# Performance work log

Hardware: AMD Instinct MI355X
Metric: run time of the kernel (lower is better)

The kernel has to match this reference:

```python
import jax, jax.numpy as jnp
import numpy as np

B_, T_, TS, DE, H, LD, OD = 16, 4096, 64, 128, 256, 512, 10
RMIN, RMAX, MAXPH = 0.9, 0.999, 6.283
EPS = 1e-5
NBLK = 6


def setup_inputs() -> dict:
    key = jax.random.key(0)
    ks = jax.random.split(key, 14)
    x = jax.random.normal(ks[0], (B_, T_, TS), jnp.float32)
    # LRU ring init (Orvieto et al.)
    u1 = jax.random.uniform(ks[1], (NBLK, H))
    u2 = jax.random.uniform(ks[2], (NBLK, H))
    nu_log = jnp.log(-0.5 * jnp.log(u1 * (RMAX**2 - RMIN**2) + RMIN**2))
    theta_log = jnp.log(MAXPH * u2)
    B_re = jax.random.normal(ks[3], (NBLK, H, DE)) / np.sqrt(2 * DE)
    B_im = jax.random.normal(ks[4], (NBLK, H, DE)) / np.sqrt(2 * DE)
    C_re = jax.random.normal(ks[5], (NBLK, DE, H)) / np.sqrt(H)
    C_im = jax.random.normal(ks[6], (NBLK, DE, H)) / np.sqrt(H)
    D_lru = jax.random.normal(ks[7], (NBLK, DE))
    W1 = jax.random.normal(ks[8], (NBLK, DE, LD)) / np.sqrt(DE)
    b1 = jnp.zeros((NBLK, LD))
    W2 = jax.random.normal(ks[9], (NBLK, LD // 2, DE)) / np.sqrt(LD // 2)
    b2 = jnp.zeros((NBLK, DE))
    bn_scale = jnp.ones((NBLK, DE))
    bn_bias = jnp.zeros((NBLK, DE))
    W_enc = jax.random.normal(ks[10], (TS, DE)) / np.sqrt(TS)
    b_enc = jnp.zeros((DE,))
    W_out = jax.random.normal(ks[11], (DE, OD)) / np.sqrt(DE)
    b_out = jnp.zeros((OD,))
    return dict(x=x, nu_log=nu_log, theta_log=theta_log, B_re=B_re, B_im=B_im,
                C_re=C_re, C_im=C_im, D_lru=D_lru, W1=W1, b1=b1, W2=W2, b2=b2,
                bn_scale=bn_scale, bn_bias=bn_bias, W_enc=W_enc, b_enc=b_enc,
                W_out=W_out, b_out=b_out)


def _lru(u, nu_log_i, theta_log_i, Bre, Bim, Cre, Cim, Dv):
    # u: [B,T,DE] float. Diagonal complex linear recurrence via associative scan.
    lam = jnp.exp(-jnp.exp(nu_log_i) + 1j * jnp.exp(theta_log_i))        # [H]
    gamma = jnp.sqrt(jnp.clip(1.0 - jnp.abs(lam) ** 2, 1e-8, None))      # [H]
    Bc = (Bre + 1j * Bim) * gamma[:, None]                               # [H,DE]
    Bu = jnp.einsum('btd,hd->bth', u.astype(jnp.complex64), Bc)          # [B,T,H]
    lam_b = jnp.broadcast_to(lam, Bu.shape)

    def binop(a, b):
        return (a[0] * b[0], a[1] * b[0] + b[1])

    _, h = jax.lax.associative_scan(binop, (lam_b, Bu), axis=1)          # [B,T,H]
    y = jnp.einsum('bth,dh->btd', h, Cre + 1j * Cim).real + u * Dv
    return y


def _bn(x, scale, bias):
    # training-mode batchnorm over (batch, time) with feature axis last
    m = x.mean(axis=(0, 1))
    v = x.var(axis=(0, 1))
    return (x - m) * jax.lax.rsqrt(v + EPS) * scale + bias


def reference(x, nu_log, theta_log, B_re, B_im, C_re, C_im, D_lru,
              W1, b1, W2, b2, bn_scale, bn_bias, W_enc, b_enc, W_out, b_out):
    h = x @ W_enc + b_enc                       # [B,T,DE]
    y = h
    for i in range(NBLK):
        z = _bn(h, bn_scale[i], bn_bias[i])
        z = _lru(z, nu_log[i], theta_log[i], B_re[i], B_im[i], C_re[i], C_im[i], D_lru[i])
        z = z @ W1[i] + b1[i]                   # [B,T,LD]
        a, b = jnp.split(z, 2, axis=-1)
        z = a * jax.nn.sigmoid(b)               # GLU
        z = z @ W2[i] + b2[i]                   # [B,T,DE]
        h = z + y                               # residual to encoder output
    pooled = h.mean(axis=1)                     # pool=True: mean over tokens
    return pooled @ W_out + b_out               # [B,OD]
```

## Files before the change

kernel.cpp:

```cpp
#include <hip/hip_runtime.h>
#include <hip/hip_fp16.h>

#define BB 16
#define TT 4096
#define TSZ 64
#define DE 128
#define HH 256
#define LDIM 512
#define ODIM 10
#define NBLKS 6
#define EPSF 1e-5f
#define NC32 128
#define NC64 64
#define NROWS (BB*TT)

typedef _Float16 f16x8 __attribute__((ext_vector_type(8)));
typedef _Float16 f16x4 __attribute__((ext_vector_type(4)));
typedef float f32x4 __attribute__((ext_vector_type(4)));
#define MFMA16(a,b,c) __builtin_amdgcn_mfma_f32_16x16x32_f16((a),(b),(c),0,0,0)

enum : size_t {
  HOFF_BG = 0,
  HOFF_WC = HOFF_BG + (size_t)NBLKS*512*128,
  HOFF_W1 = HOFF_WC + (size_t)NBLKS*128*512,
  HOFF_W2 = HOFF_W1 + (size_t)NBLKS*512*128,
  HOFF_WE = HOFF_W2 + (size_t)NBLKS*128*256,
  HTOT_HALFS = HOFF_WE + 128*64
};

enum : size_t {
  WOFF_Y     = 0,
  WOFF_H     = WOFF_Y + (size_t)NROWS*DE/2,
  WOFF_W16   = WOFF_H + (size_t)NROWS*DE/2,
  WOFF_LAM   = WOFF_W16 + (HTOT_HALFS+1)/2,
  WOFF_LAML  = WOFF_LAM + (size_t)NBLKS*HH*2,
  WOFF_SL    = WOFF_LAML + (size_t)NBLKS*HH*2,
  WOFF_CARRY = WOFF_SL + (size_t)BB*NC32*HH*2,
  WOFF_STATS = WOFF_CARRY + (size_t)BB*NC32*HH*2,
  WOFF_POOL  = WOFF_STATS + (size_t)(NBLKS+1)*2*DE,
  WOFF_BU    = WOFF_POOL + (size_t)BB*DE,
  WS_FLOATS  = WOFF_BU + (size_t)BB*NC32*512*32/2
};

__global__ __launch_bounds__(256) void k_prep(
    const float* __restrict__ nu_log, const float* __restrict__ theta_log,
    const float* __restrict__ B_re, const float* __restrict__ B_im,
    const float* __restrict__ C_re, const float* __restrict__ C_im,
    const float* __restrict__ W1g, const float* __restrict__ W2g,
    const float* __restrict__ Wenc, float* __restrict__ ws)
{
  const int i = blockIdx.x, h = threadIdx.x;
  __half* w16 = (__half*)(ws + WOFF_W16);
  const float nu  = expf(nu_log[i*HH+h]);
  const float th  = expf(theta_log[i*HH+h]);
  const float mod = expf(-nu);
  const float lr = mod*cosf(th), li = mod*sinf(th);
  const float gamma = sqrtf(fmaxf(1.0f - mod*mod, 1e-8f));
  ws[WOFF_LAM + ((size_t)i*HH+h)*2+0] = lr;
  ws[WOFF_LAM + ((size_t)i*HH+h)*2+1] = li;
  {
    float ar = lr, ai = li;
    #pragma unroll
    for (int q = 0; q < 5; q++) { float nr=ar*ar-ai*ai, ni=2.0f*ar*ai; ar=nr; ai=ni; }
    ws[WOFF_LAML + ((size_t)i*HH+h)*2+0] = ar;
    ws[WOFF_LAML + ((size_t)i*HH+h)*2+1] = ai;
  }
  {
    __half* bg = w16 + HOFF_BG + (size_t)i*512*128;
    const float* bre = B_re + ((size_t)i*HH+h)*DE;
    const float* bim = B_im + ((size_t)i*HH+h)*DE;
    for (int d = 0; d < DE; d++) {
      bg[(size_t)h*128 + d]       = __float2half(bre[d]*gamma);
      bg[(size_t)(256+h)*128 + d] = __float2half(bim[d]*gamma);
    }
  }
  {
    __half* wc = w16 + HOFF_WC + (size_t)i*128*512;
    const float* cre = C_re + (size_t)i*DE*HH;
    const float* cim = C_im + (size_t)i*DE*HH;
    for (int d = 0; d < DE; d++) {
      wc[(size_t)d*512 + h]       = __float2half( cre[(size_t)d*HH + h]);
      wc[(size_t)d*512 + 256 + h] = __float2half(-cim[(size_t)d*HH + h]);
    }
  }
  {
    __half* w1t = w16 + HOFF_W1 + (size_t)i*512*128;
    for (int d = 0; d < DE; d++) {
      w1t[(size_t)h*128 + d]       = __float2half(W1g[((size_t)i*DE + d)*LDIM + h]);
      w1t[(size_t)(256+h)*128 + d] = __float2half(W1g[((size_t)i*DE + d)*LDIM + 256 + h]);
    }
  }
  if (h < 128) {
    __half* w2t = w16 + HOFF_W2 + (size_t)i*128*256;
    for (int g = 0; g < 256; g++)
      w2t[(size_t)h*256 + g] = __float2half(W2g[((size_t)i*256 + g)*DE + h]);
  }
  if (i == 0 && h < 128) {
    __half* wet = w16 + HOFF_WE;
    for (int k = 0; k < TSZ; k++)
      wet[(size_t)h*TSZ + k] = __float2half(Wenc[(size_t)k*DE + h]);
  }
}

__global__ __launch_bounds__(512) void k_enc(
    const float* __restrict__ x, const float* __restrict__ benc, float* __restrict__ ws)
{
  __shared__ __half XT[64*72];
  const int tid = threadIdx.x, w = tid >> 6, l = tid & 63;
  const size_t row0 = (size_t)blockIdx.x * 64;
  {
    const float4* xg = (const float4*)(x + row0*TSZ);
    for (int idx = tid; idx < 1024; idx += 512) {
      float4 v = xg[idx];
      const int r = idx >> 4, c4 = (idx & 15)*4;
      *(__half2*)&XT[r*72 + c4]     = __half2{__float2half(v.x), __float2half(v.y)};
      *(__half2*)&XT[r*72 + c4 + 2] = __half2{__float2half(v.z), __float2half(v.w)};
    }
  }
  __syncthreads();
  const __half* wet = (const __half*)(ws + WOFF_W16) + HOFF_WE;
  const int n0 = w*16;
  f32x4 acc[4];
  #pragma unroll
  for (int mt = 0; mt < 4; mt++) acc[mt] = (f32x4)(0.0f);
  #pragma unroll
  for (int k0 = 0; k0 < 64; k0 += 32) {
    f16x8 bf = *(const f16x8*)&wet[(size_t)(n0 + (l&15))*64 + k0 + (l>>4)*8];
    #pragma unroll
    for (int mt = 0; mt < 4; mt++) {
      f16x8 af = *(const f16x8*)&XT[(mt*16 + (l&15))*72 + k0 + (l>>4)*8];
      acc[mt] = MFMA16(af, bf, acc[mt]);
    }
  }
  const int d = n0 + (l&15);
  const float be = benc[d];
  float s = 0.0f, ss = 0.0f;
  __half* y = (__half*)(ws + WOFF_Y);
  #pragma unroll
  for (int mt = 0; mt < 4; mt++)
    #pragma unroll
    for (int j = 0; j < 4; j++) {
      const int t = mt*16 + (l>>4)*4 + j;
      const float v = acc[mt][j] + be;
      y[(row0 + t)*DE + d] = __float2half(v);
      s += v; ss += v*v;
    }
  s  += __shfl_xor(s, 16);  s  += __shfl_xor(s, 32);
  ss += __shfl_xor(ss, 16); ss += __shfl_xor(ss, 32);
  if (l < 16) {
    atomicAdd(ws + WOFF_STATS + d, s);
    atomicAdd(ws + WOFF_STATS + DE + d, ss);
  }
}

__global__ __launch_bounds__(512, 4) void k_A(
    const __half* __restrict__ hin, float* __restrict__ ws,
    const float* __restrict__ bnsg, const float* __restrict__ bnbg, int iblk)
{
  __shared__ float AC[256];
  __shared__ __half U[64*136];
  const int tid = threadIdx.x, w = tid >> 6, l = tid & 63, q = l >> 4, r = l & 15;
  const int b = blockIdx.y, cb = blockIdx.x;
  const int row0 = b*TT + cb*64;
  if (tid < 128) {
    const float inv = 1.0f / (float)NROWS;
    const float s  = ws[WOFF_STATS + ((size_t)iblk*2+0)*DE + tid];
    const float sq = ws[WOFF_STATS + ((size_t)iblk*2+1)*DE + tid];
    const float mean = s*inv;
    const float var  = sq*inv - mean*mean;
    const float a = rsqrtf(var + EPSF) * bnsg[iblk*DE + tid];
    AC[tid]       = a;
    AC[128 + tid] = bnbg[iblk*DE + tid] - mean*a;
  }
  __syncthreads();
  {
    const int row = tid >> 3, d0 = (tid & 7)*16;
    const f16x8* hp = (const f16x8*)(hin + (size_t)(row0+row)*DE + d0);
    f16x8 h0 = hp[0], h1 = hp[1];
    f16x8 u0, u1;
    #pragma unroll
    for (int j = 0; j < 8; j++) {
      u0[j] = (_Float16)((float)h0[j]*AC[d0+j]   + AC[128+d0+j]);
      u1[j] = (_Float16)((float)h1[j]*AC[d0+8+j] + AC[128+d0+8+j]);
    }
    *(f16x8*)&U[row*136 + d0]     = u0;
    *(f16x8*)&U[row*136 + d0 + 8] = u1;
  }
  __syncthreads();
  const __half* BG = (const __half*)(ws + WOFF_W16) + HOFF_BG + (size_t)iblk*512*128;
  const int n0 = w*64;
  f32x4 acc[4][4];
  #pragma unroll
  for (int mt = 0; mt < 4; mt++)
    #pragma unroll
    for (int nt = 0; nt < 4; nt++) acc[mt][nt] = (f32x4)(0.0f);
  #pragma unroll
  for (int k0 = 0; k0 < 128; k0 += 32) {
    f16x8 af[4], bf[4];
    #pragma unroll
    for (int mt = 0; mt < 4; mt++)
      af[mt] = *(const f16x8*)&U[(mt*16 + r)*136 + k0 + q*8];
    #pragma unroll
    for (int nt = 0; nt < 4; nt++)
      bf[nt] = *(const f16x8*)&BG[(size_t)(n0 + nt*16 + r)*128 + k0 + q*8];
    #pragma unroll
    for (int mt = 0; mt < 4; mt++)
      #pragma unroll
      for (int nt = 0; nt < 4; nt++)
        acc[mt][nt] = MFMA16(af[mt], bf[nt], acc[mt][nt]);
  }
  __half* bu = (__half*)(ws + WOFF_BU);
  #pragma unroll
  for (int mt = 0; mt < 4; mt++)
    #pragma unroll
    for (int nt = 0; nt < 4; nt++) {
      f16x4 pk;
      pk[0] = (_Float16)acc[mt][nt][0];
      pk[1] = (_Float16)acc[mt][nt][1];
      pk[2] = (_Float16)acc[mt][nt][2];
      pk[3] = (_Float16)acc[mt][nt][3];
      const int hc = n0 + nt*16 + r;
      __half* dst = bu + ((((size_t)b*NC32 + cb*2 + (mt>>1))*512 + hc)*32 + (mt&1)*16 + q*4);
      *(f16x4*)dst = pk;
    }
}

__global__ __launch_bounds__(256) void k_pre(float* __restrict__ ws, int iblk)
{
  const int h = threadIdx.x, c = blockIdx.x, b = blockIdx.y;
  const __half* bu = (const __half*)(ws + WOFF_BU) + ((size_t)(b*NC32 + c)*512)*32;
  f16x8 re[4], im[4];
  #pragma unroll
  for (int k = 0; k < 4; k++) {
    re[k] = *(const f16x8*)(bu + (size_t)h*32 + k*8);
    im[k] = *(const f16x8*)(bu + (size_t)(256+h)*32 + k*8);
  }
  const float lr = ws[WOFF_LAM + ((size_t)iblk*HH+h)*2+0];
  const float li = ws[WOFF_LAM + ((size_t)iblk*HH+h)*2+1];
  float sr = 0.0f, si = 0.0f;
  #pragma unroll
  for (int t = 0; t < 32; t++) {
    const float br = (float)re[t>>3][t&7];
    const float bi = (float)im[t>>3][t&7];
    const float nr = lr*sr - li*si + br;
    const float ni = lr*si + li*sr + bi;
    sr = nr; si = ni;
  }
  ws[WOFF_SL + ((size_t)(b*NC32+c)*HH + h)*2+0] = sr;
  ws[WOFF_SL + ((size_t)(b*NC32+c)*HH + h)*2+1] = si;
}

__global__ void k_carry(float* __restrict__ ws, int i)
{
  const int h = threadIdx.x;
  const int b = blockIdx.x;
  const float Lr = ws[WOFF_LAML + ((size_t)i*HH+h)*2+0];
  const float Li = ws[WOFF_LAML + ((size_t)i*HH+h)*2+1];
  float2* C = (float2*)(ws + WOFF_CARRY) + (size_t)b*NC32*HH + h;
  const float2* S = (const float2*)(ws + WOFF_SL) + (size_t)b*NC32*HH + h;
  float sr = 0.0f, si = 0.0f;
  C[0] = float2{0.0f, 0.0f};
  for (int c = 1; c < NC32; c++) {
    const float2 sl = S[(size_t)(c-1)*HH];
    const float nr = Lr*sr - Li*si + sl.x;
    const float ni = Lr*si + Li*sr + sl.y;
    sr = nr; si = ni;
    C[(size_t)c*HH] = float2{sr, si};
  }
}

__global__ __launch_bounds__(512, 4) void k_BC(
    const __half* __restrict__ hin, float* __restrict__ ws,
    const float* __restrict__ bnsg, const float* __restrict__ bnbg,
    const float* __restrict__ b1g, const float* __restrict__ b2g,
    const float* __restrict__ Dvg, int iblk, int islast)
{
  __shared__ __half HT[64*264];
  __shared__ __half YL[64*136];
  __shared__ float AC[256];
  __shared__ float DVs[128];
  const int tid = threadIdx.x, w = tid >> 6, l = tid & 63, q = l >> 4, r = l & 15;
  const int b = blockIdx.y, cb = blockIdx.x;
  const int row0 = b*TT + cb*64;
  const __half* w16 = (const __half*)(ws + WOFF_W16);

  if (tid < 128) {
    const float inv = 1.0f / (float)NROWS;
    const float s  = ws[WOFF_STATS + ((size_t)iblk*2+0)*DE + tid];
    const float sq = ws[WOFF_STATS + ((size_t)iblk*2+1)*DE + tid];
    const float mean = s*inv;
    const float var  = sq*inv - mean*mean;
    const float a = rsqrtf(var + EPSF) * bnsg[iblk*DE + tid];
    AC[tid]       = a;
    AC[128 + tid] = bnbg[iblk*DE + tid] - mean*a;
    DVs[tid] = Dvg[iblk*DE + tid];
  }

  __half2 simv[16];
  {
    const int h = tid & 255, p = tid >> 8;
    const int c32 = cb*2 + p;
    const float2 carry = *((const float2*)(ws + WOFF_CARRY) + ((size_t)b*NC32 + c32)*HH + h);
    const __half* bu = (const __half*)(ws + WOFF_BU) + ((size_t)(b*NC32 + c32)*512)*32;
    f16x8 re[4], im[4];
    #pragma unroll
    for (int k = 0; k < 4; k++) {
      re[k] = *(const f16x8*)(bu + (size_t)h*32 + k*8);
      im[k] = *(const f16x8*)(bu + (size_t)(256+h)*32 + k*8);
    }
    const float lr = ws[WOFF_LAM + ((size_t)iblk*HH+h)*2+0];
    const float li = ws[WOFF_LAM + ((size_t)iblk*HH+h)*2+1];
    float sr = carry.x, si = carry.y;
    #pragma unroll
    for (int t = 0; t < 32; t++) {
      const float br = (float)re[t>>3][t&7];
      const float bi = (float)im[t>>3][t&7];
      const float nr = lr*sr - li*si + br;
      const float ni = lr*si + li*sr + bi;
      sr = nr; si = ni;
      HT[(p*32 + t)*264 + h] = __float2half(sr);
      if ((t & 1) == 0) simv[t>>1].x = __float2half(si);
      else              simv[t>>1].y = __float2half(si);
    }
  }
  __syncthreads();

  const __half* WC = w16 + HOFF_WC + (size_t)iblk*128*512;
  const int d = w*16 + r;
  f32x4 acc2[4];
  #pragma unroll
  for (int mt = 0; mt < 4; mt++) acc2[mt] = (f32x4)(0.0f);
  #pragma unroll
  for (int k0 = 0; k0 < 256; k0 += 32) {
    f16x8 bf = *(const f16x8*)&WC[(size_t)d*512 + k0 + q*8];
    #pragma unroll
    for (int mt = 0; mt < 4; mt++) {
      f16x8 af = *(const f16x8*)&HT[(mt*16 + r)*264 + k0 + q*8];
      acc2[mt] = MFMA16(af, bf, acc2[mt]);
    }
  }
  __syncthreads();
  {
    const int h = tid & 255, p = tid >> 8;
    #pragma unroll
    for (int t = 0; t < 32; t++)
      HT[(p*32 + t)*264 + h] = ((t & 1) ? simv[t>>1].y : simv[t>>1].x);
  }
  __syncthreads();
  #pragma unroll
  for (int k0 = 0; k0 < 256; k0 += 32) {
    f16x8 bf = *(const f16x8*)&WC[(size_t)d*512 + 256 + k0 + q*8];
    #pragma unroll
    for (int mt = 0; mt < 4; mt++) {
      f16x8 af = *(const f16x8*)&HT[(mt*16 + r)*264 + k0 + q*8];
      acc2[mt] = MFMA16(af, bf, acc2[mt]);
    }
  }
  {
    const float dv = DVs[d], a = AC[d], c = AC[128+d];
    #pragma unroll
    for (int mt = 0; mt < 4; mt++)
      #pragma unroll
      for (int j = 0; j < 4; j++) {
        const int t = mt*16 + q*4 + j;
        const float u = (float)hin[(size_t)(row0+t)*DE + d]*a + c;
        YL[t*136 + d] = __float2half(acc2[mt][j] + u*dv);
      }
  }
  __syncthreads();

  {
    const __half* W1T = w16 + HOFF_W1 + (size_t)iblk*512*128;
    #pragma unroll
    for (int nt = 0; nt < 2; nt++) {
      const int ca = w*32 + nt*16 + r;
      f32x4 aa[4], ab[4];
      #pragma unroll
      for (int mt = 0; mt < 4; mt++) { aa[mt] = (f32x4)(0.0f); ab[mt] = (f32x4)(0.0f); }
      #pragma unroll
      for (int k0 = 0; k0 < 128; k0 += 32) {
        f16x8 ba = *(const f16x8*)&W1T[(size_t)ca*128 + k0 + q*8];
        f16x8 bb = *(const f16x8*)&W1T[(size_t)(256+ca)*128 + k0 + q*8];
        #pragma unroll
        for (int mt = 0; mt < 4; mt++) {
          f16x8 af = *(const f16x8*)&YL[(mt*16 + r)*136 + k0 + q*8];
          aa[mt] = MFMA16(af, ba, aa[mt]);
          ab[mt] = MFMA16(af, bb, ab[mt]);
        }
      }
      const float b1a = b1g[(size_t)iblk*LDIM + ca];
      const float b1b = b1g[(size_t)iblk*LDIM + 256 + ca];
      #pragma unroll
      for (int mt = 0; mt < 4; mt++)
        #pragma unroll
        for (int j = 0; j < 4; j++) {
          const int t = mt*16 + q*4 + j;
          const float av = aa[mt][j] + b1a;
          const float bv = ab[mt][j] + b1b;
          HT[t*264 + ca] = __float2half(av / (1.0f + __expf(-bv)));
        }
    }
  }
  __syncthreads();

  {
    const __half* W2T = w16 + HOFF_W2 + (size_t)iblk*128*256;
    f32x4 ac4[4];
    #pragma unroll
    for (int mt = 0; mt < 4; mt++) ac4[mt] = (f32x4)(0.0f);
    #pragma unroll
    for (int k0 = 0; k0 < 256; k0 += 32) {
      f16x8 bf = *(const f16x8*)&W2T[(size_t)d*256 + k0 + q*8];
      #pragma unroll
      for (int mt = 0; mt < 4; mt++) {
        f16x8 af = *(const f16x8*)&HT[(mt*16 + r)*264 + k0 + q*8];
        ac4[mt] = MFMA16(af, bf, ac4[mt]);
      }
    }
    const __half* yh = (const __half*)(ws + WOFF_Y);
    __half* hh = (__half*)(ws + WOFF_H);
    const float bb2 = b2g[(size_t)iblk*DE + d];
    float s = 0.0f, ss = 0.0f;
    #pragma unroll
    for (int mt = 0; mt < 4; mt++)
      #pragma unroll
      for (int j = 0; j < 4; j++) {
        const int t = mt*16 + q*4 + j;
        const size_t row = (size_t)(row0 + t);
        const float v = ac4[mt][j] + bb2 + (float)yh[row*DE + d];
        hh[row*DE + d] = __float2half(v);
        s += v; ss += v*v;
      }
    s  += __shfl_xor(s, 16);  s  += __shfl_xor(s, 32);
    ss += __shfl_xor(ss, 16); ss += __shfl_xor(ss, 32);
    if (l < 16) {
      atomicAdd(ws + WOFF_STATS + (size_t)((iblk+1)*2 + 0)*DE + d, s);
      atomicAdd(ws + WOFF_STATS + (size_t)((iblk+1)*2 + 1)*DE + d, ss);
      if (islast) atomicAdd(ws + WOFF_POOL + (size_t)b*DE + d, s);
    }
  }
}

__global__ void k_out(const float* __restrict__ Wout, const float* __restrict__ bout,
                      const float* __restrict__ ws, float* __restrict__ out)
{
  const int tid = threadIdx.x;
  if (tid < BB*ODIM) {
    const int b = tid / ODIM, o = tid % ODIM;
    float acc = bout[o];
    const float* p = ws + WOFF_POOL + (size_t)b*DE;
    const float invT = 1.0f / (float)TT;
    for (int d = 0; d < DE; d++) acc += p[d]*invT*Wout[d*ODIM + o];
    out[tid] = acc;
  }
}

extern "C" void kernel_launch(void* const* d_in, const int* in_sizes, int n_in,
                              void* d_out, int out_size, void* d_ws, size_t ws_size,
                              hipStream_t stream)
{
  const float* x   = (const float*)d_in[0];
  const float* nu  = (const float*)d_in[1];
  const float* th  = (const float*)d_in[2];
  const float* Bre = (const float*)d_in[3];
  const float* Bim = (const float*)d_in[4];
  const float* Cre = (const float*)d_in[5];
  const float* Cim = (const float*)d_in[6];
  const float* Dv  = (const float*)d_in[7];
  const float* W1  = (const float*)d_in[8];
  const float* b1  = (const float*)d_in[9];
  const float* W2  = (const float*)d_in[10];
  const float* b2  = (const float*)d_in[11];
  const float* bns = (const float*)d_in[12];
  const float* bnb = (const float*)d_in[13];
  const float* We  = (const float*)d_in[14];
  const float* be  = (const float*)d_in[15];
  const float* Wo  = (const float*)d_in[16];
  const float* bo  = (const float*)d_in[17];
  float* ws = (float*)d_ws;
  float* out = (float*)d_out;

  hipMemsetAsync(ws + WOFF_STATS, 0,
                 (size_t)(((NBLKS+1)*2*DE) + BB*DE)*sizeof(float), stream);

  k_prep<<<NBLKS, 256, 0, stream>>>(nu, th, Bre, Bim, Cre, Cim, W1, W2, We, ws);
  k_enc<<<NROWS/64, 512, 0, stream>>>(x, be, ws);

  const __half* Yh = (const __half*)(ws + WOFF_Y);
  const __half* Hh = (const __half*)(ws + WOFF_H);
  for (int i = 0; i < NBLKS; i++) {
    const __half* hin = (i == 0) ? Yh : Hh;
    k_A    <<<dim3(NC64, BB), 512, 0, stream>>>(hin, ws, bns, bnb, i);
    k_pre  <<<dim3(NC32, BB), 256, 0, stream>>>(ws, i);
    k_carry<<<BB, 256, 0, stream>>>(ws, i);
    k_BC   <<<dim3(NC64, BB), 512, 0, stream>>>(hin, ws, bns, bnb, b1, b2, Dv, i,
                                                (i == NBLKS-1) ? 1 : 0);
  }
  k_out<<<1, 256, 0, stream>>>(Wo, bo, ws, out);
}
```

Before: 958.8 us.

## Fuse chunk-local scan sums into k_A via lambda powers; halve k_BC tile

Drops the k_pre kernel. Each 32-step chunk's local scan endpoint is now computed inside k_A as a weighted sum of the MFMA outputs with precomputed lambda powers (lambda^(31-tau)), using cross-lane shuffles and a shared-memory reduction. k_BC now processes 32 rows per block instead of 64, with twice as many blocks and occupancy hint 6. It runs the real and imaginary halves of the state as one K=512 MFMA pass instead of two passes with an LDS rewrite, and prefetches inputs early. This saves a launch and a BU reread, at the cost of extra FMA and register work in k_A, different fp32 summation order, and more blocks reloading weights.

```diff
diff --git a/kernel.cpp b/kernel.cpp
--- a/kernel.cpp
+++ b/kernel.cpp
@@ -34,7 +34,8 @@
   WOFF_W16   = WOFF_H + (size_t)NROWS*DE/2,
   WOFF_LAM   = WOFF_W16 + (HTOT_HALFS+1)/2,
   WOFF_LAML  = WOFF_LAM + (size_t)NBLKS*HH*2,
-  WOFF_SL    = WOFF_LAML + (size_t)NBLKS*HH*2,
+  WOFF_PL32  = WOFF_LAML + (size_t)NBLKS*HH*2,
+  WOFF_SL    = WOFF_PL32 + (size_t)NBLKS*32*HH*2,
   WOFF_CARRY = WOFF_SL + (size_t)BB*NC32*HH*2,
   WOFF_STATS = WOFF_CARRY + (size_t)BB*NC32*HH*2,
   WOFF_POOL  = WOFF_STATS + (size_t)(NBLKS+1)*2*DE,
@@ -66,6 +67,17 @@
     ws[WOFF_LAML + ((size_t)i*HH+h)*2+1] = ai;
   }
   {
+    float pr = 1.0f, pi = 0.0f;
+    float* P = ws + WOFF_PL32 + (size_t)i*32*HH*2;
+    for (int j = 0; j < 32; j++) {
+      const int tau = 31 - j;
+      P[((size_t)tau*HH + h)*2+0] = pr;
+      P[((size_t)tau*HH + h)*2+1] = pi;
+      const float nr = pr*lr - pi*li, ni = pr*li + pi*lr;
+      pr = nr; pi = ni;
+    }
+  }
+  {
     __half* bg = w16 + HOFF_BG + (size_t)i*512*128;
     const float* bre = B_re + ((size_t)i*HH+h)*DE;
     const float* bim = B_im + ((size_t)i*HH+h)*DE;
@@ -159,6 +171,7 @@
 {
   __shared__ float AC[256];
   __shared__ __half U[64*136];
+  __shared__ float SC[2][2][256][2];
   const int tid = threadIdx.x, w = tid >> 6, l = tid & 63, q = l >> 4, r = l & 15;
   const int b = blockIdx.y, cb = blockIdx.x;
   const int row0 = b*TT + cb*64;
@@ -223,31 +236,51 @@
       __half* dst = bu + ((((size_t)b*NC32 + cb*2 + (mt>>1))*512 + hc)*32 + (mt&1)*16 + q*4);
       *(f16x4*)dst = pk;
     }
-}
-
-__global__ __launch_bounds__(256) void k_pre(float* __restrict__ ws, int iblk)
-{
-  const int h = threadIdx.x, c = blockIdx.x, b = blockIdx.y;
-  const __half* bu = (const __half*)(ws + WOFF_BU) + ((size_t)(b*NC32 + c)*512)*32;
-  f16x8 re[4], im[4];
-  #pragma unroll
-  for (int k = 0; k < 4; k++) {
-    re[k] = *(const f16x8*)(bu + (size_t)h*32 + k*8);
-    im[k] = *(const f16x8*)(bu + (size_t)(256+h)*32 + k*8);
-  }
-  const float lr = ws[WOFF_LAM + ((size_t)iblk*HH+h)*2+0];
-  const float li = ws[WOFF_LAM + ((size_t)iblk*HH+h)*2+1];
-  float sr = 0.0f, si = 0.0f;
-  #pragma unroll
-  for (int t = 0; t < 32; t++) {
-    const float br = (float)re[t>>3][t&7];
-    const float bi = (float)im[t>>3][t&7];
-    const float nr = lr*sr - li*si + br;
-    const float ni = lr*si + li*sr + bi;
-    sr = nr; si = ni;
-  }
-  ws[WOFF_SL + ((size_t)(b*NC32+c)*HH + h)*2+0] = sr;
-  ws[WOFF_SL + ((size_t)(b*NC32+c)*HH + h)*2+1] = si;
+  {
+    const float2* PW = (const float2*)(ws + WOFF_PL32) + (size_t)iblk*32*HH;
+    float ppr[2][4], ppi[2][4];
+    #pragma unroll
+    for (int cc = 0; cc < 2; cc++)
+      #pragma unroll
+      for (int nt = 0; nt < 4; nt++) { ppr[cc][nt] = 0.0f; ppi[cc][nt] = 0.0f; }
+    #pragma unroll
+    for (int mm = 0; mm < 2; mm++)
+      #pragma unroll
+      for (int j = 0; j < 4; j++) {
+        const int tau = mm*16 + q*4 + j;
+        #pragma unroll
+        for (int nt = 0; nt < 4; nt++) {
+          const int hcol = (w&3)*64 + nt*16 + r;
+          const float2 pw = PW[(size_t)tau*HH + hcol];
+          #pragma unroll
+          for (int cc = 0; cc < 2; cc++) {
+            const float v = acc[cc*2+mm][nt][j];
+            ppr[cc][nt] += pw.x*v;
+            ppi[cc][nt] += pw.y*v;
+          }
+        }
+      }
+    #pragma unroll
+    for (int cc = 0; cc < 2; cc++)
+      #pragma unroll
+      for (int nt = 0; nt < 4; nt++) {
+        float a0 = ppr[cc][nt], a1 = ppi[cc][nt];
+        a0 += __shfl_xor(a0, 16); a0 += __shfl_xor(a0, 32);
+        a1 += __shfl_xor(a1, 16); a1 += __shfl_xor(a1, 32);
+        if (q == 0) {
+          SC[w>>2][cc][(w&3)*64 + nt*16 + r][0] = a0;
+          SC[w>>2][cc][(w&3)*64 + nt*16 + r][1] = a1;
+        }
+      }
+  }
+  __syncthreads();
+  {
+    const int cc = tid >> 8, hh2 = tid & 255;
+    const float re_ = SC[0][cc][hh2][0] - SC[1][cc][hh2][1];
+    const float im_ = SC[0][cc][hh2][1] + SC[1][cc][hh2][0];
+    float2* SLp = (float2*)(ws + WOFF_SL) + ((size_t)b*NC32 + cb*2 + cc)*HH + hh2;
+    *SLp = float2{re_, im_};
+  }
 }
 
 __global__ void k_carry(float* __restrict__ ws, int i)
@@ -269,20 +302,43 @@
   }
 }
 
-__global__ __launch_bounds__(512, 4) void k_BC(
+__global__ __launch_bounds__(512, 6) void k_BC(
     const __half* __restrict__ hin, float* __restrict__ ws,
     const float* __restrict__ bnsg, const float* __restrict__ bnbg,
     const float* __restrict__ b1g, const float* __restrict__ b2g,
     const float* __restrict__ Dvg, int iblk, int islast)
 {
-  __shared__ __half HT[64*264];
-  __shared__ __half YL[64*136];
+  __shared__ __half HT[32*520];
+  __shared__ __half YL[32*136];
   __shared__ float AC[256];
   __shared__ float DVs[128];
   const int tid = threadIdx.x, w = tid >> 6, l = tid & 63, q = l >> 4, r = l & 15;
   const int b = blockIdx.y, cb = blockIdx.x;
-  const int row0 = b*TT + cb*64;
+  const int row0 = b*TT + cb*32;
   const __half* w16 = (const __half*)(ws + WOFF_W16);
+  const int d = w*16 + r;
+  const int h = tid & 255;
+
+  f16x8 bre[4], bim[4];
+  float2 carry = float2{0.0f, 0.0f};
+  float lr = 0.0f, li = 0.0f;
+  if (tid < 256) {
+    const __half* bu = (const __half*)(ws + WOFF_BU) + ((size_t)(b*NC32 + cb)*512)*32;
+    #pragma unroll
+    for (int k = 0; k < 4; k++) {
+      bre[k] = *(const f16x8*)(bu + (size_t)h*32 + k*8);
+      bim[k] = *(const f16x8*)(bu + (size_t)(256+h)*32 + k*8);
+    }
+    carry = *((const float2*)(ws + WOFF_CARRY) + ((size_t)b*NC32 + cb)*HH + h);
+    lr = ws[WOFF_LAM + ((size_t)iblk*HH+h)*2+0];
+    li = ws[WOFF_LAM + ((size_t)iblk*HH+h)*2+1];
+  }
+  _Float16 upre[8];
+  #pragma unroll
+  for (int mt = 0; mt < 2; mt++)
+    #pragma unroll
+    for (int j = 0; j < 4; j++)
+      upre[mt*4+j] = *(const _Float16*)&hin[(size_t)(row0 + mt*16 + q*4 + j)*DE + d];
 
   if (tid < 128) {
     const float inv = 1.0f / (float)NROWS;
@@ -296,75 +352,40 @@
     DVs[tid] = Dvg[iblk*DE + tid];
   }
 
-  __half2 simv[16];
-  {
-    const int h = tid & 255, p = tid >> 8;
-    const int c32 = cb*2 + p;
-    const float2 carry = *((const float2*)(ws + WOFF_CARRY) + ((size_t)b*NC32 + c32)*HH + h);
-    const __half* bu = (const __half*)(ws + WOFF_BU) + ((size_t)(b*NC32 + c32)*512)*32;
-    f16x8 re[4], im[4];
-    #pragma unroll
-    for (int k = 0; k < 4; k++) {
-      re[k] = *(const f16x8*)(bu + (size_t)h*32 + k*8);
-      im[k] = *(const f16x8*)(bu + (size_t)(256+h)*32 + k*8);
-    }
-    const float lr = ws[WOFF_LAM + ((size_t)iblk*HH+h)*2+0];
-    const float li = ws[WOFF_LAM + ((size_t)iblk*HH+h)*2+1];
+  if (tid < 256) {
     float sr = carry.x, si = carry.y;
     #pragma unroll
     for (int t = 0; t < 32; t++) {
-      const float br = (float)re[t>>3][t&7];
-      const float bi = (float)im[t>>3][t&7];
+      const float br = (float)bre[t>>3][t&7];
+      const float bi = (float)bim[t>>3][t&7];
       const float nr = lr*sr - li*si + br;
       const float ni = lr*si + li*sr + bi;
       sr = nr; si = ni;
-      HT[(p*32 + t)*264 + h] = __float2half(sr);
-      if ((t & 1) == 0) simv[t>>1].x = __float2half(si);
-      else              simv[t>>1].y = __float2half(si);
-    }
-  }
-  __syncthreads();
-
-  const __half* WC = w16 + HOFF_WC + (size_t)iblk*128*512;
-  const int d = w*16 + r;
-  f32x4 acc2[4];
-  #pragma unroll
-  for (int mt = 0; mt < 4; mt++) acc2[mt] = (f32x4)(0.0f);
-  #pragma unroll
-  for (int k0 = 0; k0 < 256; k0 += 32) {
-    f16x8 bf = *(const f16x8*)&WC[(size_t)d*512 + k0 + q*8];
-    #pragma unroll
-    for (int mt = 0; mt < 4; mt++) {
-      f16x8 af = *(const f16x8*)&HT[(mt*16 + r)*264 + k0 + q*8];
-      acc2[mt] = MFMA16(af, bf, acc2[mt]);
-    }
-  }
-  __syncthreads();
-  {
-    const int h = tid & 255, p = tid >> 8;
-    #pragma unroll
-    for (int t = 0; t < 32; t++)
-      HT[(p*32 + t)*264 + h] = ((t & 1) ? simv[t>>1].y : simv[t>>1].x);
-  }
-  __syncthreads();
-  #pragma unroll
-  for (int k0 = 0; k0 < 256; k0 += 32) {
-    f16x8 bf = *(const f16x8*)&WC[(size_t)d*512 + 256 + k0 + q*8];
-    #pragma unroll
-    for (int mt = 0; mt < 4; mt++) {
-      f16x8 af = *(const f16x8*)&HT[(mt*16 + r)*264 + k0 + q*8];
-      acc2[mt] = MFMA16(af, bf, acc2[mt]);
-    }
-  }
-  {
+      HT[t*520 + h]       = __float2half(sr);
+      HT[t*520 + 256 + h] = __float2half(si);
+    }
+  }
+  __syncthreads();
+
+  {
+    const __half* WC = w16 + HOFF_WC + (size_t)iblk*128*512;
+    f32x4 a0 = (f32x4)(0.0f), a1 = (f32x4)(0.0f);
+    #pragma unroll
+    for (int k0 = 0; k0 < 512; k0 += 32) {
+      f16x8 bf  = *(const f16x8*)&WC[(size_t)d*512 + k0 + q*8];
+      f16x8 af0 = *(const f16x8*)&HT[(r)*520      + k0 + q*8];
+      f16x8 af1 = *(const f16x8*)&HT[(16 + r)*520 + k0 + q*8];
+      a0 = MFMA16(af0, bf, a0);
+      a1 = MFMA16(af1, bf, a1);
+    }
     const float dv = DVs[d], a = AC[d], c = AC[128+d];
     #pragma unroll
-    for (int mt = 0; mt < 4; mt++)
+    for (int mt = 0; mt < 2; mt++)
       #pragma unroll
       for (int j = 0; j < 4; j++) {
         const int t = mt*16 + q*4 + j;
-        const float u = (float)hin[(size_t)(row0+t)*DE + d]*a + c;
-        YL[t*136 + d] = __float2half(acc2[mt][j] + u*dv);
+        const float u = (float)upre[mt*4+j]*a + c;
+        YL[t*136 + d] = __float2half((mt ? a1[j] : a0[j]) + u*dv);
       }
   }
   __syncthreads();
@@ -374,15 +395,15 @@
     #pragma unroll
     for (int nt = 0; nt < 2; nt++) {
       const int ca = w*32 + nt*16 + r;
-      f32x4 aa[4], ab[4];
-      #pragma unroll
-      for (int mt = 0; mt < 4; mt++) { aa[mt] = (f32x4)(0.0f); ab[mt] = (f32x4)(0.0f); }
+      f32x4 aa[2], ab[2];
+      aa[0] = aa[1] = (f32x4)(0.0f);
+      ab[0] = ab[1] = (f32x4)(0.0f);
       #pragma unroll
       for (int k0 = 0; k0 < 128; k0 += 32) {
         f16x8 ba = *(const f16x8*)&W1T[(size_t)ca*128 + k0 + q*8];
         f16x8 bb = *(const f16x8*)&W1T[(size_t)(256+ca)*128 + k0 + q*8];
         #pragma unroll
-        for (int mt = 0; mt < 4; mt++) {
+        for (int mt = 0; mt < 2; mt++) {
           f16x8 af = *(const f16x8*)&YL[(mt*16 + r)*136 + k0 + q*8];
           aa[mt] = MFMA16(af, ba, aa[mt]);
           ab[mt] = MFMA16(af, bb, ab[mt]);
@@ -391,13 +412,13 @@
       const float b1a = b1g[(size_t)iblk*LDIM + ca];
       const float b1b = b1g[(size_t)iblk*LDIM + 256 + ca];
       #pragma unroll
-      for (int mt = 0; mt < 4; mt++)
+      for (int mt = 0; mt < 2; mt++)
         #pragma unroll
         for (int j = 0; j < 4; j++) {
           const int t = mt*16 + q*4 + j;
           const float av = aa[mt][j] + b1a;
           const float bv = ab[mt][j] + b1b;
-          HT[t*264 + ca] = __float2half(av / (1.0f + __expf(-bv)));
+          HT[t*520 + ca] = __float2half(av / (1.0f + __expf(-bv)));
         }
     }
   }
@@ -405,29 +426,26 @@
 
   {
     const __half* W2T = w16 + HOFF_W2 + (size_t)iblk*128*256;
-    f32x4 ac4[4];
-    #pragma unroll
-    for (int mt = 0; mt < 4; mt++) ac4[mt] = (f32x4)(0.0f);
+    f32x4 a0 = (f32x4)(0.0f), a1 = (f32x4)(0.0f);
     #pragma unroll
     for (int k0 = 0; k0 < 256; k0 += 32) {
-      f16x8 bf = *(const f16x8*)&W2T[(size_t)d*256 + k0 + q*8];
-      #pragma unroll
-      for (int mt = 0; mt < 4; mt++) {
-        f16x8 af = *(const f16x8*)&HT[(mt*16 + r)*264 + k0 + q*8];
-        ac4[mt] = MFMA16(af, bf, ac4[mt]);
-      }
+      f16x8 bf  = *(const f16x8*)&W2T[(size_t)d*256 + k0 + q*8];
+      f16x8 af0 = *(const f16x8*)&HT[(r)*520      + k0 + q*8];
+      f16x8 af1 = *(const f16x8*)&HT[(16 + r)*520 + k0 + q*8];
+      a0 = MFMA16(af0, bf, a0);
+      a1 = MFMA16(af1, bf, a1);
     }
     const __half* yh = (const __half*)(ws + WOFF_Y);
     __half* hh = (__half*)(ws + WOFF_H);
     const float bb2 = b2g[(size_t)iblk*DE + d];
     float s = 0.0f, ss = 0.0f;
     #pragma unroll
-    for (int mt = 0; mt < 4; mt++)
+    for (int mt = 0; mt < 2; mt++)
       #pragma unroll
       for (int j = 0; j < 4; j++) {
         const int t = mt*16 + q*4 + j;
         const size_t row = (size_t)(row0 + t);
-        const float v = ac4[mt][j] + bb2 + (float)yh[row*DE + d];
+        const float v = (mt ? a1[j] : a0[j]) + bb2 + (float)yh[row*DE + d];
         hh[row*DE + d] = __float2half(v);
         s += v; ss += v*v;
       }
@@ -491,9 +509,8 @@
   for (int i = 0; i < NBLKS; i++) {
     const __half* hin = (i == 0) ? Yh : Hh;
     k_A    <<<dim3(NC64, BB), 512, 0, stream>>>(hin, ws, bns, bnb, i);
-    k_pre  <<<dim3(NC32, BB), 256, 0, stream>>>(ws, i);
     k_carry<<<BB, 256, 0, stream>>>(ws, i);
-    k_BC   <<<dim3(NC64, BB), 512, 0, stream>>>(hin, ws, bns, bnb, b1, b2, Dv, i,
+    k_BC   <<<dim3(NC32, BB), 512, 0, stream>>>(hin, ws, bns, bnb, b1, b2, Dv, i,
                                                 (i == NBLKS-1) ? 1 : 0);
   }
   k_out<<<1, 256, 0, stream>>>(Wo, bo, ws, out);
```

After: 1.108 ms. +15.6%, slower.
